# Kernel tuning notes

Hardware: AMD Instinct MI355X
Metric: run time of the kernel (lower is better)

## Reference

```python
import jax, jax.numpy as jnp
import numpy as np


def _mha(q, k, v, num_heads):
    # q,k,v: [B, L, C] -> multi-head attention, scale = 1/sqrt(head_dim)
    B, Lq, C = q.shape
    Lk = k.shape[1]
    d = C // num_heads
    qh = q.reshape(B, Lq, num_heads, d)
    kh = k.reshape(B, Lk, num_heads, d)
    vh = v.reshape(B, Lk, num_heads, d)
    scale = 1.0 / jnp.sqrt(jnp.asarray(d, q.dtype))
    scores = jnp.einsum('blhd,bmhd->bhlm', qh, kh) * scale
    probs = jax.nn.softmax(scores, axis=-1)
    out = jnp.einsum('bhlm,bmhd->blhd', probs, vh)
    return out.reshape(B, Lq, C)


def setup_inputs() -> dict:
    key = jax.random.key(0)
    ks = jax.random.split(key, 9)
    b, n, f, l, C = 1, 4, 8, 256, 320
    s = 0.02
    return {
        'hidden_states': jax.random.normal(ks[0], (b * n * f, l, C), jnp.float32),
        'Wq': jax.random.normal(ks[1], (C, C), jnp.float32) * s,
        'Wk': jax.random.normal(ks[2], (C, C), jnp.float32) * s,
        'Wv': jax.random.normal(ks[3], (C, C), jnp.float32) * s,
        'Wo': jax.random.normal(ks[4], (C, C), jnp.float32) * s,
        'bo': jnp.zeros((C,), jnp.float32),
        'Wq_i2v': jax.random.normal(ks[5], (C, C), jnp.float32) * s,
        'Wo_i2v': jax.random.normal(ks[6], (C, C), jnp.float32) * s,
        'bo_i2v': jnp.zeros((C,), jnp.float32),
        'num_heads': 8,
        'num_views': 4,
        'num_frames': 8,
    }


def reference(hidden_states, Wq, Wk, Wv, Wo, bo, Wq_i2v, Wo_i2v, bo_i2v,
              num_heads, num_views, num_frames):
    BNF, l, C = hidden_states.shape
    n, f = num_views, num_frames
    b = BNF // (n * f)
    # '(b n f) l c -> (b f) (n l) c'
    h = hidden_states.reshape(b, n, f, l, C).transpose(0, 2, 1, 3, 4).reshape(b * f, n * l, C)
    L = n * l

    q = h @ Wq
    k = h @ Wk
    v = h @ Wv

    # first-frame KV broadcast across all frames within the same b
    k_first = jnp.broadcast_to(k.reshape(b, f, L, C)[:, 0:1], (b, f, L, C)).reshape(b * f, L, C)
    v_first = jnp.broadcast_to(v.reshape(b, f, L, C)[:, 0:1], (b, f, L, C)).reshape(b * f, L, C)

    base = _mha(q, k, v, num_heads)

    q_i2v = h @ Wq_i2v
    i2v = _mha(q_i2v, k_first, v_first, num_heads)
    i2v = i2v @ Wo_i2v + bo_i2v

    out = (base + i2v) @ Wo + bo

    # '(b f) (n l) c -> (b n f) l c'
    out = out.reshape(b, f, n, l, C).transpose(0, 2, 1, 3, 4).reshape(b * n * f, l, C)
    return out
```

## Files before the change

### kernel.cpp

```cpp
#include <hip/hip_runtime.h>

#define MROWS 8192
#define CDIM  320

typedef __attribute__((ext_vector_type(8))) short bf16x8;
typedef __attribute__((ext_vector_type(4))) float f32x4;

__device__ __forceinline__ unsigned bfbits(float x) {
  union { float f; unsigned u; } a; a.f = x;
  return a.u + 0x8000u;
}
__device__ __forceinline__ unsigned pack2bf(float a, float b) {
  return (bfbits(a) >> 16) | (bfbits(b) & 0xffff0000u);
}
__device__ __forceinline__ void splitbf(float x, short& hi, short& lo) {
  unsigned hu = bfbits(x) & 0xffff0000u;
  union { unsigned u; float f; } h; h.u = hu;
  hi = (short)(hu >> 16);
  lo = (short)(bfbits(x - h.f) >> 16);
}

__device__ __forceinline__ int swizzle_row(int r) {
  int ff = r >> 10;
  int t  = r & 1023;
  int nn = t >> 8;
  int ll = t & 255;
  return nn * 2048 + ff * 256 + ll;
}

__global__ __launch_bounds__(256) void wc_kernel(
    const float* __restrict__ Woi, const float* __restrict__ Wo,
    float* __restrict__ Wc)
{
  const int r0 = blockIdx.x * 64, c0 = blockIdx.y * 64;
  __shared__ float As[64][36];
  __shared__ float Bs[32][68];
  const int tid = threadIdx.x, tx = tid & 15, ty = tid >> 4;
  float acc[4][4] = {};

  const int ra = tid >> 3, kq = (tid & 7) * 4;
  const int kb = tid >> 4, cq = (tid & 15) * 4;

  for (int k0 = 0; k0 < 320; k0 += 32) {
    float4 a1 = *(const float4*)(Woi + (size_t)(r0 + ra) * 320 + k0 + kq);
    float4 a2 = *(const float4*)(Woi + (size_t)(r0 + ra + 32) * 320 + k0 + kq);
    float4 b1 = *(const float4*)(Wo + (size_t)(k0 + kb) * 320 + c0 + cq);
    float4 b2 = *(const float4*)(Wo + (size_t)(k0 + kb + 16) * 320 + c0 + cq);
    __syncthreads();
    *(float4*)&As[ra][kq] = a1;
    *(float4*)&As[ra + 32][kq] = a2;
    *(float4*)&Bs[kb][cq] = b1;
    *(float4*)&Bs[kb + 16][cq] = b2;
    __syncthreads();
    #pragma unroll
    for (int kk = 0; kk < 32; ++kk) {
      float4 bv = *(const float4*)&Bs[kk][tx * 4];
      #pragma unroll
      for (int i = 0; i < 4; ++i) {
        float a = As[ty * 4 + i][kk];
        acc[i][0] = fmaf(a, bv.x, acc[i][0]);
        acc[i][1] = fmaf(a, bv.y, acc[i][1]);
        acc[i][2] = fmaf(a, bv.z, acc[i][2]);
        acc[i][3] = fmaf(a, bv.w, acc[i][3]);
      }
    }
  }
  #pragma unroll
  for (int i = 0; i < 4; ++i) {
    float4 v = make_float4(acc[i][0], acc[i][1], acc[i][2], acc[i][3]);
    *(float4*)(Wc + (size_t)(r0 + ty * 4 + i) * 320 + c0 + tx * 4) = v;
  }
}

__global__ __launch_bounds__(256) void pack_kernel(
    const float* __restrict__ hidden,
    const float* __restrict__ Wq, const float* __restrict__ Wk,
    const float* __restrict__ Wv, const float* __restrict__ Wqi,
    const float* __restrict__ Wo, const float* __restrict__ Wc,
    const float* __restrict__ bo, const float* __restrict__ boi,
    short* __restrict__ Ah, short* __restrict__ Al,
    short* __restrict__ WTh, short* __restrict__ WTl,
    short* __restrict__ WFh, short* __restrict__ WFl,
    float* __restrict__ bc, float qscale)
{
  const int b = blockIdx.x, tid = threadIdx.x;
  if (b < 64) {
    const int r0 = b * 128;
    for (int e = tid; e < 128 * 80; e += 256) {
      int r = e / 80, cq = (e % 80) * 4;
      float4 x = *(const float4*)(hidden + (size_t)swizzle_row(r0 + r) * 320 + cq);
      union { ushort4 v; short s[4]; } h, l;
      splitbf(x.x, h.s[0], l.s[0]); splitbf(x.y, h.s[1], l.s[1]);
      splitbf(x.z, h.s[2], l.s[2]); splitbf(x.w, h.s[3], l.s[3]);
      *(ushort4*)&Ah[(size_t)(r0 + r) * 320 + cq] = h.v;
      *(ushort4*)&Al[(size_t)(r0 + r) * 320 + cq] = l.v;
    }
  } else if (b < 128) {
    const int t2 = b - 64, wi = t2 >> 4, seg = t2 & 15;
    const float* W = wi == 0 ? Wq : wi == 1 ? Wk : wi == 2 ? Wv : Wqi;
    const float s = (wi == 0 || wi == 3) ? qscale : 1.0f;
    short* th = WTh + (size_t)wi * 320 * 320;
    short* tl = WTl + (size_t)wi * 320 * 320;
    for (int e = tid; e < 20 * 320; e += 256) {
      int n = seg * 20 + e / 320, k = e % 320;
      short hi, lo;
      splitbf(W[(size_t)k * 320 + n] * s, hi, lo);
      th[(size_t)n * 320 + k] = hi;
      tl[(size_t)n * 320 + k] = lo;
    }
  } else if (b < 160) {
    const int t2 = b - 128;
    for (int e = tid; e < 10 * 640; e += 256) {
      int n = t2 * 10 + e / 640, k = e % 640;
      float x = (k < 320) ? Wo[(size_t)k * 320 + n] : Wc[(size_t)(k - 320) * 320 + n];
      short hi, lo;
      splitbf(x, hi, lo);
      WFh[(size_t)n * 640 + k] = hi;
      WFl[(size_t)n * 640 + k] = lo;
    }
  } else {
    const int n = (b - 160) * 40 + tid;
    if (tid < 40) {
      float s = bo[n];
      for (int j = 0; j < 320; ++j) s = fmaf(boi[j], Wo[(size_t)j * 320 + n], s);
      bc[n] = s;
    }
  }
}

__global__ __launch_bounds__(256, 3) void mfma_gemm(
    const short* __restrict__ Ah, const short* __restrict__ Al,
    const short* __restrict__ BTh, const short* __restrict__ BTl,
    int K, int mode,
    short* __restrict__ O0, short* __restrict__ O1,
    short* __restrict__ O2, short* __restrict__ O3,
    float* __restrict__ Of, const float* __restrict__ bias)
{
  const int tid  = threadIdx.x;
  const int wave = tid >> 6;
  const int lane = tid & 63;
  const int quad = lane >> 4;
  const int l16  = lane & 15;
  const int row0 = blockIdx.x * 128;

  const short *bth, *btl;
  short* Obf = nullptr;
  int nbase, vtrans = 0;
  if (mode == 0) {
    const int ct = blockIdx.y, wi = ct / 5, cs = ct % 5;
    bth = BTh + (size_t)wi * 320 * 320;
    btl = BTl + (size_t)wi * 320 * 320;
    nbase = cs * 64;
    Obf = wi == 0 ? O0 : wi == 1 ? O1 : wi == 2 ? O2 : O3;
    vtrans = (wi == 2);
  } else {
    bth = BTh; btl = BTl;
    nbase = blockIdx.y * 64;
  }

  __shared__ short Ash[128][40], Asl[128][40];
  __shared__ short Bsh[64][40],  Bsl[64][40];

  f32x4 acc[2][4];
  #pragma unroll
  for (int mt = 0; mt < 2; ++mt)
    #pragma unroll
    for (int nt = 0; nt < 4; ++nt) acc[mt][nt] = (f32x4){0.f, 0.f, 0.f, 0.f};

  const int ar = tid >> 2, akc = (tid & 3) * 8;
  const int bn = tid >> 2, bkc = (tid & 3) * 8;

  const short* pa_h = Ah + (size_t)(row0 + ar) * K + akc;
  const short* pa_l = Al + (size_t)(row0 + ar) * K + akc;
  const short* pb_h = bth + (size_t)(nbase + bn) * K + bkc;
  const short* pb_l = btl + (size_t)(nbase + bn) * K + bkc;

  for (int k0 = 0; k0 < K; k0 += 32) {
    uint4 ah1 = *(const uint4*)(pa_h + k0);
    uint4 ah2 = *(const uint4*)(pa_h + (size_t)64 * K + k0);
    uint4 al1 = *(const uint4*)(pa_l + k0);
    uint4 al2 = *(const uint4*)(pa_l + (size_t)64 * K + k0);
    uint4 bh  = *(const uint4*)(pb_h + k0);
    uint4 bl  = *(const uint4*)(pb_l + k0);
    __syncthreads();
    *(uint4*)&Ash[ar][akc]      = ah1;
    *(uint4*)&Ash[ar + 64][akc] = ah2;
    *(uint4*)&Asl[ar][akc]      = al1;
    *(uint4*)&Asl[ar + 64][akc] = al2;
    *(uint4*)&Bsh[bn][bkc]      = bh;
    *(uint4*)&Bsl[bn][bkc]      = bl;
    __syncthreads();

    bf16x8 afh[2], afl[2], bfh[4], bfl[4];
    #pragma unroll
    for (int mt = 0; mt < 2; ++mt) {
      afh[mt] = *(const bf16x8*)&Ash[wave * 32 + mt * 16 + l16][quad * 8];
      afl[mt] = *(const bf16x8*)&Asl[wave * 32 + mt * 16 + l16][quad * 8];
    }
    #pragma unroll
    for (int nt = 0; nt < 4; ++nt) {
      bfh[nt] = *(const bf16x8*)&Bsh[nt * 16 + l16][quad * 8];
      bfl[nt] = *(const bf16x8*)&Bsl[nt * 16 + l16][quad * 8];
    }
    #pragma unroll
    for (int mt = 0; mt < 2; ++mt)
      #pragma unroll
      for (int nt = 0; nt < 4; ++nt) {
        acc[mt][nt] = __builtin_amdgcn_mfma_f32_16x16x32_bf16(afh[mt], bfh[nt], acc[mt][nt], 0, 0, 0);
        acc[mt][nt] = __builtin_amdgcn_mfma_f32_16x16x32_bf16(afh[mt], bfl[nt], acc[mt][nt], 0, 0, 0);
        acc[mt][nt] = __builtin_amdgcn_mfma_f32_16x16x32_bf16(afl[mt], bfh[nt], acc[mt][nt], 0, 0, 0);
      }
  }

  if (mode == 0) {
    if (vtrans) {
      #pragma unroll
      for (int mt = 0; mt < 2; ++mt)
        #pragma unroll
        for (int nt = 0; nt < 4; ++nt) {
          const int col  = nbase + nt * 16 + l16;
          const int rowb = row0 + wave * 32 + mt * 16 + quad * 4;
          union { ushort4 v; short s[4]; } pk;
          #pragma unroll
          for (int r = 0; r < 4; ++r) pk.s[r] = (short)(bfbits(acc[mt][nt][r]) >> 16);
          *(ushort4*)&Obf[(size_t)col * MROWS + rowb] = pk.v;
        }
    } else {
      #pragma unroll
      for (int mt = 0; mt < 2; ++mt)
        #pragma unroll
        for (int nt = 0; nt < 4; ++nt) {
          const int col  = nbase + nt * 16 + l16;
          const int rowb = row0 + wave * 32 + mt * 16 + quad * 4;
          #pragma unroll
          for (int r = 0; r < 4; ++r)
            Obf[(size_t)(rowb + r) * CDIM + col] = (short)(bfbits(acc[mt][nt][r]) >> 16);
        }
    }
  } else {
    #pragma unroll
    for (int mt = 0; mt < 2; ++mt)
      #pragma unroll
      for (int nt = 0; nt < 4; ++nt) {
        const int col  = nbase + nt * 16 + l16;
        const int rowb = row0 + wave * 32 + mt * 16 + quad * 4;
        const float bb = bias[col];
        #pragma unroll
        for (int r = 0; r < 4; ++r)
          Of[(size_t)swizzle_row(rowb + r) * CDIM + col] = acc[mt][nt][r] + bb;
      }
  }
}

__global__ __launch_bounds__(256, 4) void attn_kernel(
    const short* __restrict__ Qb, const short* __restrict__ Qi,
    const short* __restrict__ K,  const short* __restrict__ Vtg,
    short* __restrict__ AOh, short* __restrict__ AOl)
{
  const int qblk = blockIdx.x;
  const int hh   = blockIdx.y;
  const int zz   = blockIdx.z;
  const int var  = zz >> 3;
  const int bf   = zz & 7;
  const int tid  = threadIdx.x;
  const int wave = tid >> 6;
  const int lane = tid & 63;
  const int quad = lane >> 4;
  const int l16  = lane & 15;

  const short* Q = var ? Qi : Qb;
  const int kvbase = var ? 0 : (bf << 10);
  const int coff = var * 320 + hh * 40;

  __shared__ short Ks[64][72];
  __shared__ short Vt[48][72];
  __shared__ short Ps[4][2][16][72];

  if (tid < 192) {
    int row = tid / 3, cc = tid % 3;
    *(uint4*)&Ks[row][40 + cc * 8] = make_uint4(0, 0, 0, 0);
  } else {
    int t2 = tid - 192;
    *(uint4*)&Vt[40 + (t2 >> 3)][(t2 & 7) * 8] = make_uint4(0, 0, 0, 0);
  }

  const int qrow0 = (qblk << 7) + (wave << 5) + l16;
  const short* qp = Q + (size_t)((bf << 10) + qrow0) * CDIM + hh * 40;
  bf16x8 qf0[2], qf1[2];
  qf0[0] = *(const bf16x8*)(qp + quad * 8);
  qf0[1] = *(const bf16x8*)(qp + 16 * CDIM + quad * 8);
  qf1[0] = (bf16x8){0,0,0,0,0,0,0,0};
  qf1[1] = (bf16x8){0,0,0,0,0,0,0,0};
  if (quad == 0) {
    qf1[0] = *(const bf16x8*)(qp + 32);
    qf1[1] = *(const bf16x8*)(qp + 16 * CDIM + 32);
  }

  f32x4 acc[2][3];
  #pragma unroll
  for (int q = 0; q < 2; ++q)
    #pragma unroll
    for (int t = 0; t < 3; ++t) acc[q][t] = (f32x4){0.f, 0.f, 0.f, 0.f};
  float lsum[2] = {0.f, 0.f};

  const short* Kb = K   + (size_t)kvbase * CDIM + hh * 40;
  const short* Vb = Vtg + (size_t)(hh * 40) * MROWS + kvbase;

  for (int s0 = 0; s0 < 1024; s0 += 64) {
    __syncthreads();
    #pragma unroll
    for (int pass = 0; pass < 3; ++pass) {
      int uu = tid + (pass << 8);
      if (uu < 320) {
        int key = uu / 5, c = uu % 5;
        *(uint4*)&Ks[key][c * 8] =
            *(const uint4*)(Kb + (size_t)(s0 + key) * CDIM + c * 8);
      } else if (uu < 640) {
        int vv = uu - 320;
        int dcol = vv >> 3, kb2 = vv & 7;
        *(uint4*)&Vt[dcol][kb2 * 8] =
            *(const uint4*)(Vb + (size_t)dcol * MROWS + s0 + kb2 * 8);
      }
    }
    __syncthreads();

    bf16x8 kb0[4], kb1[4];
    #pragma unroll
    for (int kt = 0; kt < 4; ++kt) {
      kb0[kt] = *(const bf16x8*)&Ks[kt * 16 + l16][quad * 8];
      kb1[kt] = *(const bf16x8*)&Ks[kt * 16 + l16][32 + quad * 8];
    }

    #pragma unroll
    for (int qt = 0; qt < 2; ++qt) {
      unsigned* pr = (unsigned*)&Ps[wave][qt][l16][0];
      float ls = 0.f;
      #pragma unroll
      for (int kt = 0; kt < 4; ++kt) {
        f32x4 st = (f32x4){0.f, 0.f, 0.f, 0.f};
        st = __builtin_amdgcn_mfma_f32_16x16x32_bf16(kb0[kt], qf0[qt], st, 0, 0, 0);
        st = __builtin_amdgcn_mfma_f32_16x16x32_bf16(kb1[kt], qf1[qt], st, 0, 0, 0);
        float p0 = __expf(st[0]);
        float p1 = __expf(st[1]);
        float p2 = __expf(st[2]);
        float p3 = __expf(st[3]);
        ls += (p0 + p1) + (p2 + p3);
        pr[kt * 8 + quad * 2]     = pack2bf(p0, p1);
        pr[kt * 8 + quad * 2 + 1] = pack2bf(p2, p3);
      }
      lsum[qt] += ls;
    }

    asm volatile("s_waitcnt lgkmcnt(0)" ::: "memory");

    bf16x8 vf[2][3];
    #pragma unroll
    for (int kh = 0; kh < 2; ++kh)
      #pragma unroll
      for (int t = 0; t < 3; ++t)
        vf[kh][t] = *(const bf16x8*)&Vt[t * 16 + l16][kh * 32 + quad * 8];

    #pragma unroll
    for (int qt = 0; qt < 2; ++qt) {
      bf16x8 pa0 = *(const bf16x8*)&Ps[wave][qt][l16][quad * 8];
      bf16x8 pa1 = *(const bf16x8*)&Ps[wave][qt][l16][32 + quad * 8];
      #pragma unroll
      for (int t = 0; t < 3; ++t) {
        acc[qt][t] = __builtin_amdgcn_mfma_f32_16x16x32_bf16(pa0, vf[0][t], acc[qt][t], 0, 0, 0);
        acc[qt][t] = __builtin_amdgcn_mfma_f32_16x16x32_bf16(pa1, vf[1][t], acc[qt][t], 0, 0, 0);
      }
    }
  }

  #pragma unroll
  for (int qt = 0; qt < 2; ++qt) {
    float li = lsum[qt];
    li += __shfl_xor(li, 16);
    li += __shfl_xor(li, 32);
    float inv = 1.f / li;
    float invr[4];
    #pragma unroll
    for (int r = 0; r < 4; ++r) invr[r] = __shfl(inv, quad * 4 + r, 64);

    const int baserow = (bf << 10) + (qblk << 7) + (wave << 5) + (qt << 4) + quad * 4;
    #pragma unroll
    for (int t = 0; t < 3; ++t) {
      int dcol = t * 16 + l16;
      if (dcol < 40) {
        short* oph = AOh + (size_t)baserow * 640 + coff + dcol;
        short* opl = AOl + (size_t)baserow * 640 + coff + dcol;
        #pragma unroll
        for (int r = 0; r < 4; ++r) {
          short hi, lo;
          splitbf(acc[qt][t][r] * invr[r], hi, lo);
          oph[(size_t)r * 640] = hi;
          opl[(size_t)r * 640] = lo;
        }
      }
    }
  }
}

extern "C" void kernel_launch(void* const* d_in, const int* in_sizes, int n_in,
                              void* d_out, int out_size, void* d_ws, size_t ws_size,
                              hipStream_t stream) {
  const float* hidden  = (const float*)d_in[0];
  const float* Wq      = (const float*)d_in[1];
  const float* Wk      = (const float*)d_in[2];
  const float* Wv      = (const float*)d_in[3];
  const float* Wo      = (const float*)d_in[4];
  const float* bo      = (const float*)d_in[5];
  const float* Wq_i2v  = (const float*)d_in[6];
  const float* Wo_i2v  = (const float*)d_in[7];
  const float* bo_i2v  = (const float*)d_in[8];
  float* out = (float*)d_out;

  const size_t SZ = (size_t)MROWS * CDIM;
  short* Ah  = (short*)d_ws;
  short* Al  = Ah + SZ;
  short* qb  = Al + SZ;
  short* kb  = qb + SZ;
  short* vt  = kb + SZ;
  short* qib = vt + SZ;
  short* AOh = qib + SZ;
  short* AOl = AOh + 2 * SZ;
  short* WTh = AOl + 2 * SZ;
  short* WTl = WTh + 409600;
  short* WFh = WTl + 409600;
  short* WFl = WFh + 204800;
  float* Wc  = (float*)(WFl + 204800);
  float* bc  = Wc + 102400;

  const float qscale = 0.15811388300841898f;

  wc_kernel<<<dim3(5, 5), 256, 0, stream>>>(Wo_i2v, Wo, Wc);

  pack_kernel<<<dim3(168), 256, 0, stream>>>(
      hidden, Wq, Wk, Wv, Wq_i2v, Wo, Wc, bo, bo_i2v,
      Ah, Al, WTh, WTl, WFh, WFl, bc, qscale);

  mfma_gemm<<<dim3(64, 20), 256, 0, stream>>>(
      Ah, Al, WTh, WTl, 320, 0, qb, kb, vt, qib, nullptr, nullptr);

  attn_kernel<<<dim3(8, 8, 16), 256, 0, stream>>>(qb, qib, kb, vt, AOh, AOl);

  mfma_gemm<<<dim3(64, 5), 256, 0, stream>>>(
      AOh, AOl, WFh, WFl, 640, 1, nullptr, nullptr, nullptr, nullptr, out, bc);
}
```

Measured before the change: 217.9 us.

## Pad Q/K head dims, stream K/V from global in single-wave attention, drop AO low part

Q, K and Q_i2v are written into a buffer padded to 64 columns per head, with the pad zeroed in the pack kernel. This lets the attention kernel load full bf16x8 fragments straight from global memory with no LDS staging or block barriers. The attention kernel becomes one wave per block, with 4 query tiles each and only the P tile kept in LDS. The attention output is now stored as high bf16 only, so the output GEMM skips the low-part A loads and one of its three MFMAs. The costs are more L2 traffic for K/V, since there is no cross-wave sharing, and lower precision in the final projection.

```diff
diff --git a/kernel.cpp b/kernel.cpp
--- a/kernel.cpp
+++ b/kernel.cpp
@@ -2,6 +2,7 @@
 
 #define MROWS 8192
 #define CDIM  320
+#define QPAD  512
 
 typedef __attribute__((ext_vector_type(8))) short bf16x8;
 typedef __attribute__((ext_vector_type(4))) float f32x4;
@@ -81,7 +82,9 @@
     short* __restrict__ Ah, short* __restrict__ Al,
     short* __restrict__ WTh, short* __restrict__ WTl,
     short* __restrict__ WFh, short* __restrict__ WFl,
-    float* __restrict__ bc, float qscale)
+    float* __restrict__ bc,
+    short* __restrict__ Qp, short* __restrict__ Kp, short* __restrict__ Qip,
+    float qscale)
 {
   const int b = blockIdx.x, tid = threadIdx.x;
   if (b < 64) {
@@ -118,13 +121,22 @@
       WFh[(size_t)n * 640 + k] = hi;
       WFl[(size_t)n * 640 + k] = lo;
     }
-  } else {
+  } else if (b < 168) {
     const int n = (b - 160) * 40 + tid;
     if (tid < 40) {
       float s = bo[n];
       for (int j = 0; j < 320; ++j) s = fmaf(boi[j], Wo[(size_t)j * 320 + n], s);
       bc[n] = s;
     }
+  } else {
+    const int bz = b - 168, buf = bz >> 5, seg = bz & 31;
+    short* P = buf == 0 ? Qp : buf == 1 ? Kp : Qip;
+    const uint4 z = make_uint4(0, 0, 0, 0);
+    for (int e = tid; e < 256 * 24; e += 256) {
+      int row = (seg << 8) + (e / 24);
+      int cc = e % 24, h = cc / 3, c3 = cc % 3;
+      *(uint4*)&P[(size_t)row * QPAD + h * 64 + 40 + c3 * 8] = z;
+    }
   }
 }
 
@@ -132,8 +144,8 @@
     const short* __restrict__ Ah, const short* __restrict__ Al,
     const short* __restrict__ BTh, const short* __restrict__ BTl,
     int K, int mode,
-    short* __restrict__ O0, short* __restrict__ O1,
-    short* __restrict__ O2, short* __restrict__ O3,
+    short* __restrict__ Qp, short* __restrict__ Kp,
+    short* __restrict__ Vt, short* __restrict__ Qip,
     float* __restrict__ Of, const float* __restrict__ bias)
 {
   const int tid  = threadIdx.x;
@@ -144,15 +156,13 @@
   const int row0 = blockIdx.x * 128;
 
   const short *bth, *btl;
-  short* Obf = nullptr;
-  int nbase, vtrans = 0;
+  int nbase, wi = 0;
   if (mode == 0) {
-    const int ct = blockIdx.y, wi = ct / 5, cs = ct % 5;
+    const int ct = blockIdx.y;
+    wi = ct / 5;
     bth = BTh + (size_t)wi * 320 * 320;
     btl = BTl + (size_t)wi * 320 * 320;
-    nbase = cs * 64;
-    Obf = wi == 0 ? O0 : wi == 1 ? O1 : wi == 2 ? O2 : O3;
-    vtrans = (wi == 2);
+    nbase = (ct % 5) * 64;
   } else {
     bth = BTh; btl = BTl;
     nbase = blockIdx.y * 64;
@@ -171,31 +181,36 @@
   const int bn = tid >> 2, bkc = (tid & 3) * 8;
 
   const short* pa_h = Ah + (size_t)(row0 + ar) * K + akc;
-  const short* pa_l = Al + (size_t)(row0 + ar) * K + akc;
+  const short* pa_l = Al ? Al + (size_t)(row0 + ar) * K + akc : nullptr;
   const short* pb_h = bth + (size_t)(nbase + bn) * K + bkc;
   const short* pb_l = btl + (size_t)(nbase + bn) * K + bkc;
 
   for (int k0 = 0; k0 < K; k0 += 32) {
     uint4 ah1 = *(const uint4*)(pa_h + k0);
     uint4 ah2 = *(const uint4*)(pa_h + (size_t)64 * K + k0);
-    uint4 al1 = *(const uint4*)(pa_l + k0);
-    uint4 al2 = *(const uint4*)(pa_l + (size_t)64 * K + k0);
-    uint4 bh  = *(const uint4*)(pb_h + k0);
-    uint4 bl  = *(const uint4*)(pb_l + k0);
+    uint4 al1, al2;
+    if (Al) {
+      al1 = *(const uint4*)(pa_l + k0);
+      al2 = *(const uint4*)(pa_l + (size_t)64 * K + k0);
+    }
+    uint4 bh = *(const uint4*)(pb_h + k0);
+    uint4 bl = *(const uint4*)(pb_l + k0);
     __syncthreads();
     *(uint4*)&Ash[ar][akc]      = ah1;
     *(uint4*)&Ash[ar + 64][akc] = ah2;
-    *(uint4*)&Asl[ar][akc]      = al1;
-    *(uint4*)&Asl[ar + 64][akc] = al2;
-    *(uint4*)&Bsh[bn][bkc]      = bh;
-    *(uint4*)&Bsl[bn][bkc]      = bl;
+    if (Al) {
+      *(uint4*)&Asl[ar][akc]      = al1;
+      *(uint4*)&Asl[ar + 64][akc] = al2;
+    }
+    *(uint4*)&Bsh[bn][bkc] = bh;
+    *(uint4*)&Bsl[bn][bkc] = bl;
     __syncthreads();
 
     bf16x8 afh[2], afl[2], bfh[4], bfl[4];
     #pragma unroll
     for (int mt = 0; mt < 2; ++mt) {
       afh[mt] = *(const bf16x8*)&Ash[wave * 32 + mt * 16 + l16][quad * 8];
-      afl[mt] = *(const bf16x8*)&Asl[wave * 32 + mt * 16 + l16][quad * 8];
+      if (Al) afl[mt] = *(const bf16x8*)&Asl[wave * 32 + mt * 16 + l16][quad * 8];
     }
     #pragma unroll
     for (int nt = 0; nt < 4; ++nt) {
@@ -208,12 +223,13 @@
       for (int nt = 0; nt < 4; ++nt) {
         acc[mt][nt] = __builtin_amdgcn_mfma_f32_16x16x32_bf16(afh[mt], bfh[nt], acc[mt][nt], 0, 0, 0);
         acc[mt][nt] = __builtin_amdgcn_mfma_f32_16x16x32_bf16(afh[mt], bfl[nt], acc[mt][nt], 0, 0, 0);
-        acc[mt][nt] = __builtin_amdgcn_mfma_f32_16x16x32_bf16(afl[mt], bfh[nt], acc[mt][nt], 0, 0, 0);
+        if (Al)
+          acc[mt][nt] = __builtin_amdgcn_mfma_f32_16x16x32_bf16(afl[mt], bfh[nt], acc[mt][nt], 0, 0, 0);
       }
   }
 
   if (mode == 0) {
-    if (vtrans) {
+    if (wi == 2) {
       #pragma unroll
       for (int mt = 0; mt < 2; ++mt)
         #pragma unroll
@@ -223,18 +239,21 @@
           union { ushort4 v; short s[4]; } pk;
           #pragma unroll
           for (int r = 0; r < 4; ++r) pk.s[r] = (short)(bfbits(acc[mt][nt][r]) >> 16);
-          *(ushort4*)&Obf[(size_t)col * MROWS + rowb] = pk.v;
+          *(ushort4*)&Vt[(size_t)col * MROWS + rowb] = pk.v;
         }
     } else {
+      short* Op = wi == 0 ? Qp : wi == 1 ? Kp : Qip;
       #pragma unroll
       for (int mt = 0; mt < 2; ++mt)
         #pragma unroll
         for (int nt = 0; nt < 4; ++nt) {
           const int col  = nbase + nt * 16 + l16;
+          const int h    = col / 40;
+          const int pcol = h * 64 + (col - h * 40);
           const int rowb = row0 + wave * 32 + mt * 16 + quad * 4;
           #pragma unroll
           for (int r = 0; r < 4; ++r)
-            Obf[(size_t)(rowb + r) * CDIM + col] = (short)(bfbits(acc[mt][nt][r]) >> 16);
+            Op[(size_t)(rowb + r) * QPAD + pcol] = (short)(bfbits(acc[mt][nt][r]) >> 16);
         }
     }
   } else {
@@ -252,88 +271,57 @@
   }
 }
 
-__global__ __launch_bounds__(256, 4) void attn_kernel(
-    const short* __restrict__ Qb, const short* __restrict__ Qi,
-    const short* __restrict__ K,  const short* __restrict__ Vtg,
-    short* __restrict__ AOh, short* __restrict__ AOl)
+__global__ __launch_bounds__(64, 2) void attn_kernel(
+    const short* __restrict__ Qp, const short* __restrict__ Qip,
+    const short* __restrict__ Kp, const short* __restrict__ Vtg,
+    short* __restrict__ AOh)
 {
   const int qblk = blockIdx.x;
   const int hh   = blockIdx.y;
   const int zz   = blockIdx.z;
   const int var  = zz >> 3;
   const int bf   = zz & 7;
-  const int tid  = threadIdx.x;
-  const int wave = tid >> 6;
-  const int lane = tid & 63;
+  const int lane = threadIdx.x;
   const int quad = lane >> 4;
   const int l16  = lane & 15;
 
-  const short* Q = var ? Qi : Qb;
+  const short* Q = var ? Qip : Qp;
   const int kvbase = var ? 0 : (bf << 10);
   const int coff = var * 320 + hh * 40;
 
-  __shared__ short Ks[64][72];
-  __shared__ short Vt[48][72];
-  __shared__ short Ps[4][2][16][72];
-
-  if (tid < 192) {
-    int row = tid / 3, cc = tid % 3;
-    *(uint4*)&Ks[row][40 + cc * 8] = make_uint4(0, 0, 0, 0);
-  } else {
-    int t2 = tid - 192;
-    *(uint4*)&Vt[40 + (t2 >> 3)][(t2 & 7) * 8] = make_uint4(0, 0, 0, 0);
-  }
-
-  const int qrow0 = (qblk << 7) + (wave << 5) + l16;
-  const short* qp = Q + (size_t)((bf << 10) + qrow0) * CDIM + hh * 40;
-  bf16x8 qf0[2], qf1[2];
-  qf0[0] = *(const bf16x8*)(qp + quad * 8);
-  qf0[1] = *(const bf16x8*)(qp + 16 * CDIM + quad * 8);
-  qf1[0] = (bf16x8){0,0,0,0,0,0,0,0};
-  qf1[1] = (bf16x8){0,0,0,0,0,0,0,0};
-  if (quad == 0) {
-    qf1[0] = *(const bf16x8*)(qp + 32);
-    qf1[1] = *(const bf16x8*)(qp + 16 * CDIM + 32);
-  }
-
-  f32x4 acc[2][3];
+  __shared__ short Ps[4][16][72];
+
+  bf16x8 qf0[4], qf1[4];
   #pragma unroll
-  for (int q = 0; q < 2; ++q)
-    #pragma unroll
-    for (int t = 0; t < 3; ++t) acc[q][t] = (f32x4){0.f, 0.f, 0.f, 0.f};
-  float lsum[2] = {0.f, 0.f};
-
-  const short* Kb = K   + (size_t)kvbase * CDIM + hh * 40;
+  for (int qt = 0; qt < 4; ++qt) {
+    const short* qp = Q + (size_t)((bf << 10) + (qblk << 6) + (qt << 4) + l16) * QPAD + hh * 64;
+    qf0[qt] = *(const bf16x8*)(qp + quad * 8);
+    qf1[qt] = *(const bf16x8*)(qp + 32 + quad * 8);
+  }
+
+  f32x4 acc[4][3];
+  float lsum[4];
+  #pragma unroll
+  for (int qt = 0; qt < 4; ++qt) {
+    lsum[qt] = 0.f;
+    #pragma unroll
+    for (int t = 0; t < 3; ++t) acc[qt][t] = (f32x4){0.f, 0.f, 0.f, 0.f};
+  }
+
+  const short* Kb = Kp + (size_t)kvbase * QPAD + hh * 64;
   const short* Vb = Vtg + (size_t)(hh * 40) * MROWS + kvbase;
 
   for (int s0 = 0; s0 < 1024; s0 += 64) {
-    __syncthreads();
-    #pragma unroll
-    for (int pass = 0; pass < 3; ++pass) {
-      int uu = tid + (pass << 8);
-      if (uu < 320) {
-        int key = uu / 5, c = uu % 5;
-        *(uint4*)&Ks[key][c * 8] =
-            *(const uint4*)(Kb + (size_t)(s0 + key) * CDIM + c * 8);
-      } else if (uu < 640) {
-        int vv = uu - 320;
-        int dcol = vv >> 3, kb2 = vv & 7;
-        *(uint4*)&Vt[dcol][kb2 * 8] =
-            *(const uint4*)(Vb + (size_t)dcol * MROWS + s0 + kb2 * 8);
-      }
-    }
-    __syncthreads();
-
     bf16x8 kb0[4], kb1[4];
     #pragma unroll
     for (int kt = 0; kt < 4; ++kt) {
-      kb0[kt] = *(const bf16x8*)&Ks[kt * 16 + l16][quad * 8];
-      kb1[kt] = *(const bf16x8*)&Ks[kt * 16 + l16][32 + quad * 8];
-    }
-
-    #pragma unroll
-    for (int qt = 0; qt < 2; ++qt) {
-      unsigned* pr = (unsigned*)&Ps[wave][qt][l16][0];
+      const short* kp = Kb + (size_t)(s0 + kt * 16 + l16) * QPAD;
+      kb0[kt] = *(const bf16x8*)(kp + quad * 8);
+      kb1[kt] = *(const bf16x8*)(kp + 32 + quad * 8);
+    }
+
+    #pragma unroll
+    for (int qt = 0; qt < 4; ++qt) {
       float ls = 0.f;
       #pragma unroll
       for (int kt = 0; kt < 4; ++kt) {
@@ -345,8 +333,10 @@
         float p2 = __expf(st[2]);
         float p3 = __expf(st[3]);
         ls += (p0 + p1) + (p2 + p3);
-        pr[kt * 8 + quad * 2]     = pack2bf(p0, p1);
-        pr[kt * 8 + quad * 2 + 1] = pack2bf(p2, p3);
+        uint2 pk;
+        pk.x = pack2bf(p0, p1);
+        pk.y = pack2bf(p2, p3);
+        *(uint2*)&Ps[qt][l16][kt * 16 + quad * 4] = pk;
       }
       lsum[qt] += ls;
     }
@@ -358,12 +348,12 @@
     for (int kh = 0; kh < 2; ++kh)
       #pragma unroll
       for (int t = 0; t < 3; ++t)
-        vf[kh][t] = *(const bf16x8*)&Vt[t * 16 + l16][kh * 32 + quad * 8];
-
-    #pragma unroll
-    for (int qt = 0; qt < 2; ++qt) {
-      bf16x8 pa0 = *(const bf16x8*)&Ps[wave][qt][l16][quad * 8];
-      bf16x8 pa1 = *(const bf16x8*)&Ps[wave][qt][l16][32 + quad * 8];
+        vf[kh][t] = *(const bf16x8*)(Vb + (size_t)(t * 16 + l16) * MROWS + s0 + kh * 32 + quad * 8);
+
+    #pragma unroll
+    for (int qt = 0; qt < 4; ++qt) {
+      bf16x8 pa0 = *(const bf16x8*)&Ps[qt][l16][quad * 8];
+      bf16x8 pa1 = *(const bf16x8*)&Ps[qt][l16][32 + quad * 8];
       #pragma unroll
       for (int t = 0; t < 3; ++t) {
         acc[qt][t] = __builtin_amdgcn_mfma_f32_16x16x32_bf16(pa0, vf[0][t], acc[qt][t], 0, 0, 0);
@@ -373,7 +363,7 @@
   }
 
   #pragma unroll
-  for (int qt = 0; qt < 2; ++qt) {
+  for (int qt = 0; qt < 4; ++qt) {
     float li = lsum[qt];
     li += __shfl_xor(li, 16);
     li += __shfl_xor(li, 32);
@@ -382,20 +372,15 @@
     #pragma unroll
     for (int r = 0; r < 4; ++r) invr[r] = __shfl(inv, quad * 4 + r, 64);
 
-    const int baserow = (bf << 10) + (qblk << 7) + (wave << 5) + (qt << 4) + quad * 4;
+    const int baserow = (bf << 10) + (qblk << 6) + (qt << 4) + quad * 4;
     #pragma unroll
     for (int t = 0; t < 3; ++t) {
       int dcol = t * 16 + l16;
       if (dcol < 40) {
-        short* oph = AOh + (size_t)baserow * 640 + coff + dcol;
-        short* opl = AOl + (size_t)baserow * 640 + coff + dcol;
+        short* op = AOh + (size_t)baserow * 640 + coff + dcol;
         #pragma unroll
-        for (int r = 0; r < 4; ++r) {
-          short hi, lo;
-          splitbf(acc[qt][t][r] * invr[r], hi, lo);
-          oph[(size_t)r * 640] = hi;
-          opl[(size_t)r * 640] = lo;
-        }
+        for (int r = 0; r < 4; ++r)
+          op[(size_t)r * 640] = (short)(bfbits(acc[qt][t][r] * invr[r]) >> 16);
       }
     }
   }
@@ -415,16 +400,16 @@
   const float* bo_i2v  = (const float*)d_in[8];
   float* out = (float*)d_out;
 
-  const size_t SZ = (size_t)MROWS * CDIM;
+  const size_t SZ  = (size_t)MROWS * CDIM;
+  const size_t SZP = (size_t)MROWS * QPAD;
   short* Ah  = (short*)d_ws;
   short* Al  = Ah + SZ;
-  short* qb  = Al + SZ;
-  short* kb  = qb + SZ;
-  short* vt  = kb + SZ;
-  short* qib = vt + SZ;
-  short* AOh = qib + SZ;
-  short* AOl = AOh + 2 * SZ;
-  short* WTh = AOl + 2 * SZ;
+  short* AOh = Ah;
+  short* Qp  = Al + SZ;
+  short* Kp  = Qp + SZP;
+  short* Qip = Kp + SZP;
+  short* Vt  = Qip + SZP;
+  short* WTh = Vt + (size_t)328 * MROWS;
   short* WTl = WTh + 409600;
   short* WFh = WTl + 409600;
   short* WFl = WFh + 204800;
@@ -435,15 +420,15 @@
 
   wc_kernel<<<dim3(5, 5), 256, 0, stream>>>(Wo_i2v, Wo, Wc);
 
-  pack_kernel<<<dim3(168), 256, 0, stream>>>(
+  pack_kernel<<<dim3(264), 256, 0, stream>>>(
       hidden, Wq, Wk, Wv, Wq_i2v, Wo, Wc, bo, bo_i2v,
-      Ah, Al, WTh, WTl, WFh, WFl, bc, qscale);
+      Ah, Al, WTh, WTl, WFh, WFl, bc, Qp, Kp, Qip, qscale);
 
   mfma_gemm<<<dim3(64, 20), 256, 0, stream>>>(
-      Ah, Al, WTh, WTl, 320, 0, qb, kb, vt, qib, nullptr, nullptr);
-
-  attn_kernel<<<dim3(8, 8, 16), 256, 0, stream>>>(qb, qib, kb, vt, AOh, AOl);
+      Ah, Al, WTh, WTl, 320, 0, Qp, Kp, Vt, Qip, nullptr, nullptr);
+
+  attn_kernel<<<dim3(16, 8, 16), 64, 0, stream>>>(Qp, Qip, Kp, Vt, AOh);
 
   mfma_gemm<<<dim3(64, 5), 256, 0, stream>>>(
-      AOh, AOl, WFh, WFl, 640, 1, nullptr, nullptr, nullptr, nullptr, out, bc);
-}
+      AOh, nullptr, WFh, WFl, 640, 1, nullptr, nullptr, nullptr, nullptr, out, bc);
+}
```

After: 229.2 us. +5.2%, slower.
